# Performance work log

Hardware: AMD Instinct MI355X
Metric: run time of the kernel (lower is better)

The kernel has to match this reference:

```python
import jax, jax.numpy as jnp
import numpy as np

S, B, C = 7, 2, 20
LAMBDA_COORD = 5.0
LAMBDA_NOOBJ = 0.5
WH_EPS = 1e-6
IOU_EPS = 1e-6
BATCH = 16384


def _iou_yolo(a, b):
    # a, b: [..., 4] in (cx, cy, w, h) 'yolo' center format
    ax1, ay1 = a[..., 0] - a[..., 2] / 2, a[..., 1] - a[..., 3] / 2
    ax2, ay2 = a[..., 0] + a[..., 2] / 2, a[..., 1] + a[..., 3] / 2
    bx1, by1 = b[..., 0] - b[..., 2] / 2, b[..., 1] - b[..., 3] / 2
    bx2, by2 = b[..., 0] + b[..., 2] / 2, b[..., 1] + b[..., 3] / 2
    iw = jnp.clip(jnp.minimum(ax2, bx2) - jnp.maximum(ax1, bx1), 0.0)
    ih = jnp.clip(jnp.minimum(ay2, by2) - jnp.maximum(ay1, by1), 0.0)
    inter = iw * ih
    area_a = jnp.abs((ax2 - ax1) * (ay2 - ay1))
    area_b = jnp.abs((bx2 - bx1) * (by2 - by1))
    return inter / (area_a + area_b - inter + IOU_EPS)


def setup_inputs() -> dict:
    key = jax.random.key(0)
    k1, k2, k3 = jax.random.split(key, 3)
    D = C + 5 * B  # 30
    y_trues = jax.random.uniform(k1, (BATCH, S, S, D), dtype=jnp.float32)
    # conf channel must be exactly 0.0 or 1.0 (loss branches on == 1)
    conf = (jax.random.uniform(k2, (BATCH, S, S)) < 0.3).astype(jnp.float32)
    y_trues = y_trues.at[..., 4].set(conf)
    y_preds = jax.random.normal(k3, (BATCH, S, S, D), dtype=jnp.float32)
    return {"y_trues": y_trues, "y_preds": y_preds}


def reference(y_trues, y_preds):
    D = C + 5 * B
    t = y_trues.reshape(-1, S * S, D)   # [N, 49, 30]
    p = y_preds.reshape(-1, S * S, D)
    batch_size = p.shape[0]

    b = t[..., 0:4]
    bhat1 = p[..., 0:4]
    bhat2 = p[..., 5:9]

    iou1 = _iou_yolo(b, bhat1)          # [N, 49]
    iou2 = _iou_yolo(b, bhat2)
    use1 = iou1 > iou2

    bhat = jnp.where(use1[..., None], bhat1, bhat2)            # responsible box
    confhat_chosen = jnp.where(use1, p[..., 4], p[..., 9])
    confhat_other = jnp.where(use1, p[..., 9], p[..., 4])

    # coord losses (object cells)
    xy = LAMBDA_COORD * ((b[..., 0] - bhat[..., 0]) ** 2 + (b[..., 1] - bhat[..., 1]) ** 2)
    wh = LAMBDA_COORD * (
        (jnp.sqrt(b[..., 2]) - jnp.sqrt(jnp.abs(bhat[..., 2] + WH_EPS))) ** 2
        + (jnp.sqrt(b[..., 3]) - jnp.sqrt(jnp.abs(bhat[..., 3] + WH_EPS))) ** 2
    )
    obj_conf = (t[..., 4] - confhat_chosen) ** 2
    noobj_in_obj = LAMBDA_NOOBJ * (0.0 - confhat_other) ** 2
    cls = jnp.sum((t[..., 10:] - p[..., 10:]) ** 2, axis=-1)

    obj_terms = xy + wh + obj_conf + noobj_in_obj + cls

    # no-object cells: penalize both predicted confs toward y_true conf (== target conf channel)
    noobj_terms = LAMBDA_NOOBJ * (
        (t[..., 4] - p[..., 4]) ** 2 + (t[..., 4] - p[..., 9]) ** 2
    )

    obj_mask = t[..., 4] == 1.0
    total = jnp.sum(jnp.where(obj_mask, obj_terms, noobj_terms))
    return total / batch_size
```

## Files before the change

kernel.cpp:

```cpp
#include <hip/hip_runtime.h>

#define LAMBDA_COORD 5.0f
#define LAMBDA_NOOBJ 0.5f
#define WH_EPS 1e-6f
#define IOU_EPS 1e-6f

__device__ __forceinline__ float iou_yolo(float a0, float a1, float a2, float a3,
                                          float b0, float b1, float b2, float b3) {
    float ax1 = a0 - a2 * 0.5f, ay1 = a1 - a3 * 0.5f;
    float ax2 = a0 + a2 * 0.5f, ay2 = a1 + a3 * 0.5f;
    float bx1 = b0 - b2 * 0.5f, by1 = b1 - b3 * 0.5f;
    float bx2 = b0 + b2 * 0.5f, by2 = b1 + b3 * 0.5f;
    float iw = fmaxf(fminf(ax2, bx2) - fmaxf(ax1, bx1), 0.0f);
    float ih = fmaxf(fminf(ay2, by2) - fmaxf(ay1, by1), 0.0f);
    float inter = iw * ih;
    float area_a = fabsf((ax2 - ax1) * (ay2 - ay1));
    float area_b = fabsf((bx2 - bx1) * (by2 - by1));
    return inter / (area_a + area_b - inter + IOU_EPS);
}

__device__ __forceinline__ float cell_loss(const float* t, const float* p) {
    const float b0 = t[0], b1 = t[1], b2 = t[2], b3 = t[3], t4 = t[4];

    float iou1 = iou_yolo(b0, b1, b2, b3, p[0], p[1], p[2], p[3]);
    float iou2 = iou_yolo(b0, b1, b2, b3, p[5], p[6], p[7], p[8]);
    bool use1 = iou1 > iou2;

    float bh0 = use1 ? p[0] : p[5];
    float bh1 = use1 ? p[1] : p[6];
    float bh2 = use1 ? p[2] : p[7];
    float bh3 = use1 ? p[3] : p[8];
    float conf_c = use1 ? p[4] : p[9];
    float conf_o = use1 ? p[9] : p[4];

    float dx = b0 - bh0, dy = b1 - bh1;
    float xy = LAMBDA_COORD * (dx * dx + dy * dy);

    float sw = sqrtf(b2) - sqrtf(fabsf(bh2 + WH_EPS));
    float sh = sqrtf(b3) - sqrtf(fabsf(bh3 + WH_EPS));
    float wh = LAMBDA_COORD * (sw * sw + sh * sh);

    float dc = t4 - conf_c;
    float obj_conf = dc * dc;
    float noobj_in_obj = LAMBDA_NOOBJ * conf_o * conf_o;

    float cls = 0.0f;
#pragma unroll
    for (int k = 10; k < 30; ++k) {
        float d = t[k] - p[k];
        cls += d * d;
    }

    float obj_terms = xy + wh + obj_conf + noobj_in_obj + cls;

    float d4 = t4 - p[4], d9 = t4 - p[9];
    float noobj_terms = LAMBDA_NOOBJ * (d4 * d4 + d9 * d9);

    return (t4 == 1.0f) ? obj_terms : noobj_terms;
}

constexpr int CELLS = 256;
constexpr int CFLOATS = CELLS * 30;
constexpr int CVEC4 = CFLOATS / 4;
constexpr int NITER = CVEC4 / 256;

__global__ __launch_bounds__(256) void yolo_loss_kernel(
    const float* __restrict__ t_g, const float* __restrict__ p_g,
    float* __restrict__ out, float inv_batch) {
    __shared__ float st[CFLOATS];
    __shared__ float sp[CFLOATS];
    __shared__ float swave[4];

    const int tid = threadIdx.x;
    const size_t base4 = (size_t)blockIdx.x * CVEC4;
    const float4* tg = (const float4*)t_g + base4;
    const float4* pg = (const float4*)p_g + base4;
    float4* st4 = (float4*)st;
    float4* sp4 = (float4*)sp;

#pragma unroll
    for (int j = 0; j < NITER; ++j) {
        int i = tid + j * 256;
        st4[i] = tg[i];
        sp4[i] = pg[i];
    }
    {
        int i = tid + NITER * 256;
        if (i < CVEC4) {
            st4[i] = tg[i];
            sp4[i] = pg[i];
        }
    }
    __syncthreads();

    float v = cell_loss(st + tid * 30, sp + tid * 30);

#pragma unroll
    for (int off = 32; off > 0; off >>= 1)
        v += __shfl_down(v, off, 64);

    int lane = tid & 63;
    int wid = tid >> 6;
    if (lane == 0) swave[wid] = v;
    __syncthreads();
    if (tid == 0) {
        float s = swave[0] + swave[1] + swave[2] + swave[3];
        atomicAdd(out, s * inv_batch);
    }
}

extern "C" void kernel_launch(void* const* d_in, const int* in_sizes, int n_in,
                              void* d_out, int out_size, void* d_ws, size_t ws_size,
                              hipStream_t stream) {
    const float* t = (const float*)d_in[0];
    const float* p = (const float*)d_in[1];
    float* out = (float*)d_out;

    const int total = in_sizes[0];
    const int cells = total / 30;
    const int batch = cells / 49;
    const float inv_batch = 1.0f / (float)batch;

    hipMemsetAsync(out, 0, sizeof(float), stream);

    const int grid = cells / CELLS;
    yolo_loss_kernel<<<grid, 256, 0, stream>>>(t, p, out, inv_batch);
}
```

Before: 207.8 us.

## Stage tiles via global_load_lds in a persistent grid and split per-cell work

Replaces the register-staged copy into shared memory with direct global-to-LDS loads (global_load_lds, 16 bytes per lane), so loads skip VGPRs. The kernel becomes persistent: a fixed grid of 1280 blocks walks 128-cell chunks, which cuts the number of atomics and block launches. Within a chunk, half the threads compute the box/conf terms and the other half compute the class sum for object cells only, spreading the work across 256 threads. The trade-offs are two barriers per chunk, no overlap between loading the next chunk and computing the current one, and a dependence on a toolchain that supports the 16-byte LDS DMA builtin.

```diff
diff --git a/kernel.cpp b/kernel.cpp
--- a/kernel.cpp
+++ b/kernel.cpp
@@ -4,6 +4,11 @@
 #define LAMBDA_NOOBJ 0.5f
 #define WH_EPS 1e-6f
 #define IOU_EPS 1e-6f
+
+constexpr int CELLS   = 128;
+constexpr int CFLOATS = CELLS * 30;
+constexpr int CVEC4   = CFLOATS / 4;
+constexpr int GRID    = 1280;
 
 __device__ __forceinline__ float iou_yolo(float a0, float a1, float a2, float a3,
                                           float b0, float b1, float b2, float b3) {
@@ -19,7 +24,7 @@
     return inter / (area_a + area_b - inter + IOU_EPS);
 }
 
-__device__ __forceinline__ float cell_loss(const float* t, const float* p) {
+__device__ __forceinline__ float cell_main(const float* t, const float* p) {
     const float b0 = t[0], b1 = t[1], b2 = t[2], b3 = t[3], t4 = t[4];
 
     float iou1 = iou_yolo(b0, b1, b2, b3, p[0], p[1], p[2], p[3]);
@@ -44,14 +49,7 @@
     float obj_conf = dc * dc;
     float noobj_in_obj = LAMBDA_NOOBJ * conf_o * conf_o;
 
-    float cls = 0.0f;
-#pragma unroll
-    for (int k = 10; k < 30; ++k) {
-        float d = t[k] - p[k];
-        cls += d * d;
-    }
-
-    float obj_terms = xy + wh + obj_conf + noobj_in_obj + cls;
+    float obj_terms = xy + wh + obj_conf + noobj_in_obj;
 
     float d4 = t4 - p[4], d9 = t4 - p[9];
     float noobj_terms = LAMBDA_NOOBJ * (d4 * d4 + d9 * d9);
@@ -59,48 +57,69 @@
     return (t4 == 1.0f) ? obj_terms : noobj_terms;
 }
 
-constexpr int CELLS = 256;
-constexpr int CFLOATS = CELLS * 30;
-constexpr int CVEC4 = CFLOATS / 4;
-constexpr int NITER = CVEC4 / 256;
+__device__ __forceinline__ void stage16(const float4* g_wave, float4* l_wave, int lane) {
+    __builtin_amdgcn_global_load_lds(
+        (const __attribute__((address_space(1))) void*)(g_wave + lane),
+        (__attribute__((address_space(3))) void*)l_wave,
+        16, 0, 0);
+}
 
 __global__ __launch_bounds__(256) void yolo_loss_kernel(
     const float* __restrict__ t_g, const float* __restrict__ p_g,
-    float* __restrict__ out, float inv_batch) {
-    __shared__ float st[CFLOATS];
-    __shared__ float sp[CFLOATS];
+    float* __restrict__ out, int nchunks, float inv_batch) {
+    __shared__ float4 st4[CVEC4];
+    __shared__ float4 sp4[CVEC4];
     __shared__ float swave[4];
+    float* st = (float*)st4;
+    float* sp = (float*)sp4;
 
-    const int tid = threadIdx.x;
-    const size_t base4 = (size_t)blockIdx.x * CVEC4;
-    const float4* tg = (const float4*)t_g + base4;
-    const float4* pg = (const float4*)p_g + base4;
-    float4* st4 = (float4*)st;
-    float4* sp4 = (float4*)sp;
+    const int tid  = threadIdx.x;
+    const int lane = tid & 63;
+    const int wb   = tid - lane;
+
+    float v = 0.0f;
+
+    for (int chunk = blockIdx.x; chunk < nchunks; chunk += GRID) {
+        const float4* tg = (const float4*)t_g + (size_t)chunk * CVEC4;
+        const float4* pg = (const float4*)p_g + (size_t)chunk * CVEC4;
 
 #pragma unroll
-    for (int j = 0; j < NITER; ++j) {
-        int i = tid + j * 256;
-        st4[i] = tg[i];
-        sp4[i] = pg[i];
+        for (int j = 0; j < 3; ++j) {
+            int b = wb + j * 256;
+            stage16(tg + b, st4 + b, lane);
+            stage16(pg + b, sp4 + b, lane);
+        }
+        if (tid < 192) {
+            int b = wb + 768;
+            stage16(tg + b, st4 + b, lane);
+            stage16(pg + b, sp4 + b, lane);
+        }
+        __syncthreads();
+
+        if (tid < CELLS) {
+            v += cell_main(st + tid * 30, sp + tid * 30);
+        } else {
+            const int c = tid - CELLS;
+            const float* t = st + c * 30;
+            const float* p = sp + c * 30;
+            if (t[4] == 1.0f) {
+                float cls = 0.0f;
+#pragma unroll
+                for (int k = 10; k < 30; ++k) {
+                    float d = t[k] - p[k];
+                    cls += d * d;
+                }
+                v += cls;
+            }
+        }
+        __syncthreads();
     }
-    {
-        int i = tid + NITER * 256;
-        if (i < CVEC4) {
-            st4[i] = tg[i];
-            sp4[i] = pg[i];
-        }
-    }
-    __syncthreads();
-
-    float v = cell_loss(st + tid * 30, sp + tid * 30);
 
 #pragma unroll
     for (int off = 32; off > 0; off >>= 1)
         v += __shfl_down(v, off, 64);
 
-    int lane = tid & 63;
-    int wid = tid >> 6;
+    const int wid = tid >> 6;
     if (lane == 0) swave[wid] = v;
     __syncthreads();
     if (tid == 0) {
@@ -116,13 +135,13 @@
     const float* p = (const float*)d_in[1];
     float* out = (float*)d_out;
 
-    const int total = in_sizes[0];
-    const int cells = total / 30;
-    const int batch = cells / 49;
+    const int total  = in_sizes[0];
+    const int cells  = total / 30;
+    const int chunks = cells / CELLS;
+    const int batch  = cells / 49;
     const float inv_batch = 1.0f / (float)batch;
 
     hipMemsetAsync(out, 0, sizeof(float), stream);
 
-    const int grid = cells / CELLS;
-    yolo_loss_kernel<<<grid, 256, 0, stream>>>(t, p, out, inv_batch);
+    yolo_loss_kernel<<<GRID, 256, 0, stream>>>(t, p, out, chunks, inv_batch);
 }
```

After: 208.4 us. Within noise of the previous version (+0.3%).
